# Optimization experiments

Hardware: AMD Instinct MI355X
Metric: run time of the kernel (lower is better)

Reference implementation:

```python
import jax, jax.numpy as jnp
import numpy as np

N = 16383        # complete binary tree, 14 levels
D_NODE = 512
D_SSM = 512
D_STATE = 16
MAX_DEPTH = 14   # number of BFS levels (depth 0..13)
LN_EPS = 1e-5


def setup_inputs() -> dict:
    key = jax.random.key(0)
    ks = jax.random.split(key, 8)
    # tree structure: parent[i] = (i-1)//2, root has parent -1; BFS order == index order
    parent = np.concatenate([np.array([-1]), (np.arange(1, N) - 1) // 2]).astype(np.int64)
    depth = np.floor(np.log2(np.arange(N) + 1)).astype(np.int32)
    s = jax.random.normal(ks[0], (N, D_NODE), jnp.float32)
    w = jax.random.uniform(ks[1], (N,), jnp.float32, minval=0.01, maxval=1.0)
    # parameters (xavier-ish scales)
    W_in = jax.random.normal(ks[2], (D_SSM, D_NODE + 1), jnp.float32) * (1.0 / np.sqrt(D_NODE + 1))
    b_in = jnp.zeros((D_SSM,), jnp.float32)
    W_delta = jax.random.normal(ks[3], (D_SSM, D_SSM), jnp.float32) * (1.0 / np.sqrt(D_SSM))
    # dt-style bias init: softplus(b) ~ dt in [1e-3, 1e-1]
    dt = jnp.exp(jax.random.uniform(ks[4], (D_SSM,), jnp.float32) * (np.log(0.1) - np.log(0.001)) + np.log(0.001))
    b_delta = dt + jnp.log(-jnp.expm1(-dt))
    W_w = jax.random.normal(ks[5], (D_SSM, 1), jnp.float32)
    b_w = jnp.zeros((D_SSM,), jnp.float32)
    A_log = jnp.log(jnp.broadcast_to(jnp.arange(1.0, D_STATE + 1.0, dtype=jnp.float32)[None, :], (D_SSM, D_STATE)))
    D = jnp.ones((D_SSM,), jnp.float32)
    W_B = jax.random.normal(ks[6], (D_STATE, D_SSM), jnp.float32) * (1.0 / np.sqrt(D_SSM))
    b_B = jnp.zeros((D_STATE,), jnp.float32)
    W_C = jax.random.normal(ks[7], (D_STATE, D_SSM), jnp.float32) * (1.0 / np.sqrt(D_SSM))
    b_C = jnp.zeros((D_STATE,), jnp.float32)
    gamma = jnp.ones((D_SSM,), jnp.float32)
    beta = jnp.zeros((D_SSM,), jnp.float32)
    return {"s": s, "w": w, "parent": jnp.asarray(parent), "depth": jnp.asarray(depth),
            "W_in": W_in, "b_in": b_in, "W_delta": W_delta, "b_delta": b_delta,
            "W_w": W_w, "b_w": b_w, "A_log": A_log, "D": D,
            "W_B": W_B, "b_B": b_B, "W_C": W_C, "b_C": b_C,
            "gamma": gamma, "beta": beta}


def reference(s, w, parent, depth, W_in, b_in, W_delta, b_delta, W_w, b_w,
              A_log, D, W_B, b_B, W_C, b_C, gamma, beta):
    n = s.shape[0]
    log_w = jnp.log(w + 1e-6)[:, None]                       # [N, 1]
    feat = jnp.concatenate([s, log_w], axis=1)               # [N, d_node+1]
    x = feat @ W_in.T + b_in                                 # [N, d_ssm]
    delta = jax.nn.softplus(x @ W_delta.T + b_delta) * jax.nn.sigmoid(log_w @ W_w.T + b_w)  # [N, d_ssm]
    A = -jnp.exp(A_log)                                      # [d_ssm, d_state]
    B = x @ W_B.T + b_B                                      # [N, d_state]
    C = x @ W_C.T + b_C                                      # [N, d_state]
    A_bar = jnp.exp(delta[:, :, None] * A[None])             # [N, d_ssm, d_state]
    Bx = (delta * x)[:, :, None] * B[:, None, :]             # [N, d_ssm, d_state]
    # level-parallel tree scan: all nodes at BFS depth l updated together
    par = jnp.maximum(parent, 0)
    has_par = (parent >= 0)[:, None, None]
    H = jnp.zeros((n, A_bar.shape[1], A_bar.shape[2]), x.dtype)
    for lvl in range(MAX_DEPTH):
        h_par = jnp.where(has_par, jnp.take(H, par, axis=0), 0.0)
        H = jnp.where((depth == lvl)[:, None, None], A_bar * h_par + Bx, H)
    Y = jnp.einsum('nds,ns->nd', H, C) + D * x               # [N, d_ssm]
    mu = jnp.mean(Y, axis=-1, keepdims=True)
    var = jnp.var(Y, axis=-1, keepdims=True)
    return (Y - mu) / jnp.sqrt(var + LN_EPS) * gamma + beta
```

## Files before the change

kernel.cpp:

```cpp
#include <hip/hip_runtime.h>
#include <hip/hip_bf16.h>
#include <math.h>

#define D_SSM 512
#define D_STATE 16
#define CKPT_BASE 511
#define CKPT_END 1023
#define N_CKPT 512
#define MPAD 16384

typedef __attribute__((ext_vector_type(8))) short short8;
typedef __attribute__((ext_vector_type(4))) float floatx4;

__device__ __forceinline__ unsigned short f2bf(float f) {
    unsigned int u = __float_as_uint(f);
    unsigned int r = (u + 0x7fffu + ((u >> 16) & 1u)) >> 16;
    return (unsigned short)r;
}
__device__ __forceinline__ float bf2f(unsigned short u) {
    return __uint_as_float(((unsigned int)u) << 16);
}
__device__ __forceinline__ void g2lds16(const void* g, void* l) {
    __builtin_amdgcn_global_load_lds(
        (const __attribute__((address_space(1))) void*)g,
        (__attribute__((address_space(3))) void*)l, 16, 0, 0);
}

__global__ __launch_bounds__(256) void prep_kernel(
    const float* __restrict__ s, const float* __restrict__ w,
    const float* __restrict__ W_in, const float* __restrict__ W_delta,
    const float* __restrict__ W_B, const float* __restrict__ W_C,
    unsigned short* __restrict__ s_bf, float* __restrict__ lw,
    unsigned short* __restrict__ Win_bf, unsigned short* __restrict__ Wd_bf,
    int Nn)
{
    const int b = blockIdx.x, t = threadIdx.x;
    if (b < MPAD) {
        unsigned int pack = 0;
        if (b < Nn) {
            float2 sv = *(const float2*)(s + (size_t)b * 512 + t * 2);
            pack = (unsigned int)f2bf(sv.x) | ((unsigned int)f2bf(sv.y) << 16);
        }
        *(unsigned int*)(s_bf + (size_t)b * 512 + t * 2) = pack;
        if (t == 0) lw[b] = (b < Nn) ? logf(w[b] + 1e-6f) : 0.f;
    } else if (b < MPAD + 512) {
        int c = b - MPAD;
        float a0 = W_in[(size_t)c * 513 + t * 2];
        float a1 = W_in[(size_t)c * 513 + t * 2 + 1];
        *(unsigned int*)(Win_bf + (size_t)c * 512 + t * 2) =
            (unsigned int)f2bf(a0) | ((unsigned int)f2bf(a1) << 16);
    } else if (b < MPAD + 1024) {
        int c = b - MPAD - 512;
        float2 wv = *(const float2*)(W_delta + (size_t)c * 512 + t * 2);
        *(unsigned int*)(Wd_bf + (size_t)c * 512 + t * 2) =
            (unsigned int)f2bf(wv.x) | ((unsigned int)f2bf(wv.y) << 16);
    } else {
        int c = b - MPAD - 1024;
        float2 wv; wv.x = 0.f; wv.y = 0.f;
        if (c < 16)      wv = *(const float2*)(W_B + (size_t)c * 512 + t * 2);
        else if (c < 32) wv = *(const float2*)(W_C + (size_t)(c - 16) * 512 + t * 2);
        *(unsigned int*)(Wd_bf + (size_t)(512 + c) * 512 + t * 2) =
            (unsigned int)f2bf(wv.x) | ((unsigned int)f2bf(wv.y) << 16);
    }
}

__global__ __launch_bounds__(256) void gemm_mfma(
    const unsigned short* __restrict__ Abf,
    const unsigned short* __restrict__ Wbf,
    float* __restrict__ outf,
    unsigned short* __restrict__ outbf,
    const float* __restrict__ bias,
    const float* __restrict__ lw,
    const float* __restrict__ wcol, int wcol_stride,
    const float* __restrict__ bw,
    const float* __restrict__ b_B, const float* __restrict__ b_C,
    float* __restrict__ Bm, float* __restrict__ Cm,
    int mode)
{
    __shared__ __align__(16) short As[2][128 * 32];
    __shared__ __align__(16) short Bs[2][128 * 32];
    const int tid = threadIdx.x;
    const int wave = tid >> 6, lane = tid & 63;
    const int row0 = blockIdx.y * 128;
    const int col0 = blockIdx.x * 128;
    const int wr = (wave >> 1) * 64;
    const int wc = (wave & 1) * 64;

    floatx4 acc[4][4] = {};

    const int srow = lane >> 2;
    const int sg   = (lane & 3) ^ ((srow >> 1) & 3);
    const int scol = sg * 8;

    const unsigned short* Ag = Abf + (size_t)(row0 + wave * 16 + srow) * 512 + scol;
    const unsigned short* Wg = Wbf + (size_t)(col0 + wave * 16 + srow) * 512 + scol;
    char* Al = (char*)&As[0][0] + wave * 1024;
    char* Bl = (char*)&Bs[0][0] + wave * 1024;

    #define STAGE(buf, k0)                                              \
        do {                                                            \
            g2lds16(Ag + (k0),            Al + (buf) * 8192);           \
            g2lds16(Ag + 64 * 512 + (k0), Al + (buf) * 8192 + 4096);    \
            g2lds16(Wg + (k0),            Bl + (buf) * 8192);           \
            g2lds16(Wg + 64 * 512 + (k0), Bl + (buf) * 8192 + 4096);    \
        } while (0)

    STAGE(0, 0);
    __syncthreads();

    for (int it = 0; it < 16; ++it) {
        const int cur = it & 1;
        if (it < 15) STAGE(cur ^ 1, (it + 1) * 32);

        short8 af[4], bfr[4];
        #pragma unroll
        for (int i = 0; i < 4; i++) {
            int m = wr + i * 16 + (lane & 15);
            int gm = (lane >> 4) ^ ((m >> 1) & 3);
            af[i] = *(const short8*)&As[cur][m * 32 + gm * 8];
        }
        #pragma unroll
        for (int j = 0; j < 4; j++) {
            int n = wc + j * 16 + (lane & 15);
            int gn = (lane >> 4) ^ ((n >> 1) & 3);
            bfr[j] = *(const short8*)&Bs[cur][n * 32 + gn * 8];
        }
        #pragma unroll
        for (int i = 0; i < 4; i++)
            #pragma unroll
            for (int j = 0; j < 4; j++)
                acc[i][j] = __builtin_amdgcn_mfma_f32_16x16x32_bf16(af[i], bfr[j], acc[i][j], 0, 0, 0);
        __syncthreads();
    }
    #undef STAGE

    if (col0 >= 512) {
        #pragma unroll
        for (int i = 0; i < 4; i++) {
            #pragma unroll
            for (int reg = 0; reg < 4; reg++) {
                int r = row0 + wr + i * 16 + (lane >> 4) * 4 + reg;
                #pragma unroll
                for (int j = 0; j < 4; j++) {
                    int c2 = wc + j * 16 + (lane & 15);
                    float z = acc[i][j][reg];
                    if (c2 < 16)      Bm[(size_t)r * 16 + c2]        = z + b_B[c2];
                    else if (c2 < 32) Cm[(size_t)r * 16 + (c2 - 16)] = z + b_C[c2 - 16];
                }
            }
        }
        return;
    }

    #pragma unroll
    for (int i = 0; i < 4; i++) {
        #pragma unroll
        for (int reg = 0; reg < 4; reg++) {
            int r = row0 + wr + i * 16 + (lane >> 4) * 4 + reg;
            float lwr = lw[r];
            #pragma unroll
            for (int j = 0; j < 4; j++) {
                int c = col0 + wc + j * 16 + (lane & 15);
                float z = acc[i][j][reg] + bias[c];
                if (mode == 0) {
                    float o = z + lwr * wcol[(size_t)c * wcol_stride];
                    outbf[(size_t)r * 512 + c] = f2bf(o);
                } else {
                    float sp = (z > 15.f) ? z : __logf(1.f + __expf(z));
                    float sg2 = __builtin_amdgcn_rcpf(1.f + __expf(-(lwr * wcol[c] + bw[c])));
                    outf[(size_t)r * 512 + c] = sp * sg2;
                }
            }
        }
    }
}

__device__ __forceinline__ bool geo_check(const float* As) {
    bool ok = true;
    #pragma unroll
    for (int s = 1; s < 16; s++) {
        float want = (float)(s + 1) * As[0];
        ok = ok && (fabsf(As[s] - want) <= 1e-4f * (float)(s + 1));
    }
    return ok;
}

__global__ __launch_bounds__(256) void ckpt_kernel(
    const unsigned short* __restrict__ x_bf, const float* __restrict__ delta,
    const float* __restrict__ Bm, const float* __restrict__ A_log,
    float* __restrict__ H9)
{
    const int n9 = blockIdx.x;
    const int t = threadIdx.x;
    const int d0 = t, d1 = t + 256;

    float As0[16], As1[16], acc0[16], acc1[16];
    #pragma unroll
    for (int s = 0; s < 16; s++) {
        As0[s] = -__expf(A_log[d0 * 16 + s]);
        As1[s] = -__expf(A_log[d1 * 16 + s]);
        acc0[s] = 0.f; acc1[s] = 0.f;
    }
    const bool fast = geo_check(As0) && geo_check(As1);

    float cum0 = 0.f, cum1 = 0.f;
    int a = CKPT_BASE + n9;
    while (a >= 0) {
        float da0 = delta[(size_t)a * 512 + d0];
        float da1 = delta[(size_t)a * 512 + d1];
        float bx0 = da0 * bf2f(x_bf[(size_t)a * 512 + d0]);
        float bx1 = da1 * bf2f(x_bf[(size_t)a * 512 + d1]);
        if (fast) {
            float r0 = __expf(As0[0] * cum0);
            float r1 = __expf(As1[0] * cum1);
            float pw0 = r0, pw1 = r1;
            #pragma unroll
            for (int s = 0; s < 16; s++) {
                float Bs = Bm[a * 16 + s];
                acc0[s] = fmaf(bx0 * pw0, Bs, acc0[s]);
                acc1[s] = fmaf(bx1 * pw1, Bs, acc1[s]);
                pw0 *= r0; pw1 *= r1;
            }
        } else {
            #pragma unroll
            for (int s = 0; s < 16; s++) {
                float Bs = Bm[a * 16 + s];
                acc0[s] = fmaf(bx0 * __expf(As0[s] * cum0), Bs, acc0[s]);
                acc1[s] = fmaf(bx1 * __expf(As1[s] * cum1), Bs, acc1[s]);
            }
        }
        cum0 += da0; cum1 += da1;
        a = (a - 1) >> 1;
    }

    float* p0 = H9 + ((size_t)n9 * 512 + d0) * 16;
    float* p1 = H9 + ((size_t)n9 * 512 + d1) * 16;
    #pragma unroll
    for (int s = 0; s < 16; s++) { p0[s] = acc0[s]; p1[s] = acc1[s]; }
}

__global__ __launch_bounds__(256) void scan_shallow(
    const unsigned short* __restrict__ x_bf, const float* __restrict__ delta,
    const float* __restrict__ Bm, const float* __restrict__ Cm,
    const float* __restrict__ A_log, const float* __restrict__ Dv,
    const float* __restrict__ gamma, const float* __restrict__ beta,
    float* __restrict__ out)
{
    const int n = blockIdx.x;
    const int t = threadIdx.x;
    const int d0 = t, d1 = t + 256;

    float As0[16], As1[16], acc0[16], acc1[16];
    #pragma unroll
    for (int s = 0; s < 16; s++) {
        As0[s] = -__expf(A_log[d0 * 16 + s]);
        As1[s] = -__expf(A_log[d1 * 16 + s]);
        acc0[s] = 0.f; acc1[s] = 0.f;
    }
    const bool fast = geo_check(As0) && geo_check(As1);

    float cum0 = 0.f, cum1 = 0.f;
    int a = n;
    while (a >= 0) {
        float da0 = delta[(size_t)a * 512 + d0];
        float da1 = delta[(size_t)a * 512 + d1];
        float bx0 = da0 * bf2f(x_bf[(size_t)a * 512 + d0]);
        float bx1 = da1 * bf2f(x_bf[(size_t)a * 512 + d1]);
        if (fast) {
            float r0 = __expf(As0[0] * cum0);
            float r1 = __expf(As1[0] * cum1);
            float pw0 = r0, pw1 = r1;
            #pragma unroll
            for (int s = 0; s < 16; s++) {
                float Bs = Bm[a * 16 + s];
                acc0[s] = fmaf(bx0 * pw0, Bs, acc0[s]);
                acc1[s] = fmaf(bx1 * pw1, Bs, acc1[s]);
                pw0 *= r0; pw1 *= r1;
            }
        } else {
            #pragma unroll
            for (int s = 0; s < 16; s++) {
                float Bs = Bm[a * 16 + s];
                acc0[s] = fmaf(bx0 * __expf(As0[s] * cum0), Bs, acc0[s]);
                acc1[s] = fmaf(bx1 * __expf(As1[s] * cum1), Bs, acc1[s]);
            }
        }
        cum0 += da0; cum1 += da1;
        a = (a - 1) >> 1;
    }

    float xn0 = bf2f(x_bf[(size_t)n * 512 + d0]);
    float xn1 = bf2f(x_bf[(size_t)n * 512 + d1]);
    float y0 = Dv[d0] * xn0, y1 = Dv[d1] * xn1;
    #pragma unroll
    for (int s = 0; s < 16; s++) {
        float Cs = Cm[(size_t)n * 16 + s];
        y0 += Cs * acc0[s];
        y1 += Cs * acc1[s];
    }

    float s1 = y0 + y1;
    float s2 = y0 * y0 + y1 * y1;
    #pragma unroll
    for (int off = 32; off > 0; off >>= 1) {
        s1 += __shfl_xor(s1, off);
        s2 += __shfl_xor(s2, off);
    }
    __shared__ float red[8];
    int wid = t >> 6, lane = t & 63;
    if (lane == 0) { red[wid] = s1; red[wid + 4] = s2; }
    __syncthreads();
    float S1 = red[0] + red[1] + red[2] + red[3];
    float S2 = red[4] + red[5] + red[6] + red[7];
    float mu = S1 * (1.f / 512.f);
    float var = S2 * (1.f / 512.f) - mu * mu;
    float inv = rsqrtf(var + 1e-5f);
    out[(size_t)n * 512 + d0] = (y0 - mu) * inv * gamma[d0] + beta[d0];
    out[(size_t)n * 512 + d1] = (y1 - mu) * inv * gamma[d1] + beta[d1];
}

__global__ __launch_bounds__(512) void scan_deep(
    const unsigned short* __restrict__ x_bf, const float* __restrict__ delta,
    const float* __restrict__ Bm, const float* __restrict__ Cm,
    const float* __restrict__ H9,
    const float* __restrict__ A_log, const float* __restrict__ Dv,
    const float* __restrict__ gamma, const float* __restrict__ beta,
    float* __restrict__ out)
{
    __shared__ float Y[31][512];
    __shared__ int nid[31];
    const int p = blockIdx.x;
    const int d = threadIdx.x;
    const int a9 = CKPT_BASE + p;

    float As0 = -__expf(A_log[d * 16]);
    bool fast = true;
    #pragma unroll
    for (int s = 1; s < 16; s++) {
        float As = -__expf(A_log[d * 16 + s]);
        fast = fast && (fabsf(As - (float)(s + 1) * As0) <= 1e-4f * (float)(s + 1));
    }

    float H9v[16];
    #pragma unroll
    for (int s = 0; s < 16; s++) H9v[s] = H9[((size_t)p * 512 + d) * 16 + s];

    {
        float xv = bf2f(x_bf[(size_t)a9 * 512 + d]);
        float y = Dv[d] * xv;
        #pragma unroll
        for (int s = 0; s < 16; s++) y = fmaf(Cm[(size_t)a9 * 16 + s], H9v[s], y);
        Y[0][d] = y;
        if (d == 0) nid[0] = a9;
    }

    auto step = [&](int n, const float* Hp, float* Hc, int slot) {
        float dlt = delta[(size_t)n * 512 + d];
        float xv = bf2f(x_bf[(size_t)n * 512 + d]);
        float bx = dlt * xv;
        const float* Bn = Bm + (size_t)n * 16;
        const float* Cn = Cm + (size_t)n * 16;
        float y = Dv[d] * xv;
        if (fast) {
            float r = __expf(As0 * dlt);
            float pw = r;
            #pragma unroll
            for (int s = 0; s < 16; s++) {
                Hc[s] = fmaf(pw, Hp[s], bx * Bn[s]);
                y = fmaf(Cn[s], Hc[s], y);
                pw *= r;
            }
        } else {
            #pragma unroll
            for (int s = 0; s < 16; s++) {
                float Ab = __expf(dlt * (-__expf(A_log[d * 16 + s])));
                Hc[s] = fmaf(Ab, Hp[s], bx * Bn[s]);
                y = fmaf(Cn[s], Hc[s], y);
            }
        }
        Y[slot][d] = y;
        if (d == 0) nid[slot] = n;
    };

    float H10[16], H11[16], H12[16], H13[16];
    int slot = 1;
    #pragma unroll
    for (int c0 = 0; c0 < 2; c0++) {
        int n10 = 2 * a9 + 1 + c0;
        step(n10, H9v, H10, slot++);
        #pragma unroll
        for (int c1 = 0; c1 < 2; c1++) {
            int n11 = 2 * n10 + 1 + c1;
            step(n11, H10, H11, slot++);
            #pragma unroll
            for (int c2 = 0; c2 < 2; c2++) {
                int n12 = 2 * n11 + 1 + c2;
                step(n12, H11, H12, slot++);
                #pragma unroll
                for (int c3 = 0; c3 < 2; c3++) {
                    int n13 = 2 * n12 + 1 + c3;
                    step(n13, H12, H13, slot++);
                }
            }
        }
    }
    __syncthreads();

    const int w = d >> 6, lane = d & 63;
    for (int i = w; i < 31; i += 8) {
        int n = nid[i];
        float v[8]; float s1 = 0.f, s2 = 0.f;
        #pragma unroll
        for (int k = 0; k < 8; k++) {
            v[k] = Y[i][lane + 64 * k];
            s1 += v[k]; s2 += v[k] * v[k];
        }
        #pragma unroll
        for (int off = 32; off > 0; off >>= 1) {
            s1 += __shfl_xor(s1, off);
            s2 += __shfl_xor(s2, off);
        }
        float mu = s1 * (1.f / 512.f);
        float inv = rsqrtf(s2 * (1.f / 512.f) - mu * mu + 1e-5f);
        #pragma unroll
        for (int k = 0; k < 8; k++) {
            int ch = lane + 64 * k;
            out[(size_t)n * 512 + ch] = (v[k] - mu) * inv * gamma[ch] + beta[ch];
        }
    }
}

extern "C" void kernel_launch(void* const* d_in, const int* in_sizes, int n_in,
                              void* d_out, int out_size, void* d_ws, size_t ws_size,
                              hipStream_t stream) {
    const float* s_in   = (const float*)d_in[0];
    const float* w      = (const float*)d_in[1];
    const float* W_in    = (const float*)d_in[4];
    const float* b_in    = (const float*)d_in[5];
    const float* W_delta = (const float*)d_in[6];
    const float* b_delta = (const float*)d_in[7];
    const float* W_w     = (const float*)d_in[8];
    const float* b_w     = (const float*)d_in[9];
    const float* A_log   = (const float*)d_in[10];
    const float* Dv      = (const float*)d_in[11];
    const float* W_B     = (const float*)d_in[12];
    const float* b_B     = (const float*)d_in[13];
    const float* W_C     = (const float*)d_in[14];
    const float* b_C     = (const float*)d_in[15];
    const float* gamma   = (const float*)d_in[16];
    const float* beta    = (const float*)d_in[17];
    float* out = (float*)d_out;

    const int Nn = in_sizes[1];

    float* ws    = (float*)d_ws;
    float* lw    = ws;
    float* delta = lw + MPAD;
    float* Bm    = delta + (size_t)MPAD * 512;
    float* Cm    = Bm + (size_t)MPAD * 16;
    float* H9    = Cm + (size_t)MPAD * 16;
    unsigned short* s_bf  = (unsigned short*)(H9 + (size_t)N_CKPT * 512 * 16);
    unsigned short* x_bf  = s_bf + (size_t)MPAD * 512;
    unsigned short* Win_bf = x_bf + (size_t)MPAD * 512;
    unsigned short* Wd_bf  = Win_bf + 512 * 512;

    prep_kernel<<<MPAD + 1024 + 128, 256, 0, stream>>>(s_in, w, W_in, W_delta, W_B, W_C,
                                                       s_bf, lw, Win_bf, Wd_bf, Nn);

    dim3 g1(4, 128);
    gemm_mfma<<<g1, 256, 0, stream>>>(s_bf, Win_bf, nullptr, x_bf,
                                      b_in, lw, W_in + 512, 513, nullptr,
                                      nullptr, nullptr, nullptr, nullptr, 0);
    dim3 g2(5, 128);
    gemm_mfma<<<g2, 256, 0, stream>>>(x_bf, Wd_bf, delta, nullptr,
                                      b_delta, lw, W_w, 1, b_w,
                                      b_B, b_C, Bm, Cm, 1);

    ckpt_kernel<<<N_CKPT, 256, 0, stream>>>(x_bf, delta, Bm, A_log, H9);

    scan_shallow<<<CKPT_BASE, 256, 0, stream>>>(x_bf, delta, Bm, Cm, A_log, Dv,
                                                gamma, beta, out);

    scan_deep<<<N_CKPT, 512, 0, stream>>>(x_bf, delta, Bm, Cm, H9, A_log, Dv,
                                          gamma, beta, out);
}
```

Measured before the change: 244.0 us.

## Fuse checkpoint computation into scan_deep and swizzle GEMM workgroup order

Removes the separate ckpt_kernel that wrote per-checkpoint states H9 to global memory; scan_deep now walks the ancestor chain itself to build the depth-9 state in registers. This drops one launch and the H9 write/read round trip (512x512x16 floats). Separately, the GEMM remaps block indices with an XCD-aware swizzle so neighbouring tiles land on the same chiplet for better L2 reuse. The fused path uses one thread per channel with 512 threads, so the ancestor walk's latency now sits in front of the deep scan rather than running as its own kernel.

```diff
diff --git a/kernel.cpp b/kernel.cpp
--- a/kernel.cpp
+++ b/kernel.cpp
@@ -5,7 +5,6 @@
 #define D_SSM 512
 #define D_STATE 16
 #define CKPT_BASE 511
-#define CKPT_END 1023
 #define N_CKPT 512
 #define MPAD 16384
 
@@ -81,8 +80,15 @@
     __shared__ __align__(16) short Bs[2][128 * 32];
     const int tid = threadIdx.x;
     const int wave = tid >> 6, lane = tid & 63;
-    const int row0 = blockIdx.y * 128;
-    const int col0 = blockIdx.x * 128;
+
+    const int nwg  = gridDim.x * gridDim.y;
+    const int orig = blockIdx.y * gridDim.x + blockIdx.x;
+    const int wsw  = (orig & 7) * (nwg >> 3) + (orig >> 3);
+    const int bx   = wsw % gridDim.x;
+    const int by   = wsw / gridDim.x;
+    const int row0 = by * 128;
+    const int col0 = bx * 128;
+
     const int wr = (wave >> 1) * 64;
     const int wc = (wave & 1) * 64;
 
@@ -185,60 +191,6 @@
     return ok;
 }
 
-__global__ __launch_bounds__(256) void ckpt_kernel(
-    const unsigned short* __restrict__ x_bf, const float* __restrict__ delta,
-    const float* __restrict__ Bm, const float* __restrict__ A_log,
-    float* __restrict__ H9)
-{
-    const int n9 = blockIdx.x;
-    const int t = threadIdx.x;
-    const int d0 = t, d1 = t + 256;
-
-    float As0[16], As1[16], acc0[16], acc1[16];
-    #pragma unroll
-    for (int s = 0; s < 16; s++) {
-        As0[s] = -__expf(A_log[d0 * 16 + s]);
-        As1[s] = -__expf(A_log[d1 * 16 + s]);
-        acc0[s] = 0.f; acc1[s] = 0.f;
-    }
-    const bool fast = geo_check(As0) && geo_check(As1);
-
-    float cum0 = 0.f, cum1 = 0.f;
-    int a = CKPT_BASE + n9;
-    while (a >= 0) {
-        float da0 = delta[(size_t)a * 512 + d0];
-        float da1 = delta[(size_t)a * 512 + d1];
-        float bx0 = da0 * bf2f(x_bf[(size_t)a * 512 + d0]);
-        float bx1 = da1 * bf2f(x_bf[(size_t)a * 512 + d1]);
-        if (fast) {
-            float r0 = __expf(As0[0] * cum0);
-            float r1 = __expf(As1[0] * cum1);
-            float pw0 = r0, pw1 = r1;
-            #pragma unroll
-            for (int s = 0; s < 16; s++) {
-                float Bs = Bm[a * 16 + s];
-                acc0[s] = fmaf(bx0 * pw0, Bs, acc0[s]);
-                acc1[s] = fmaf(bx1 * pw1, Bs, acc1[s]);
-                pw0 *= r0; pw1 *= r1;
-            }
-        } else {
-            #pragma unroll
-            for (int s = 0; s < 16; s++) {
-                float Bs = Bm[a * 16 + s];
-                acc0[s] = fmaf(bx0 * __expf(As0[s] * cum0), Bs, acc0[s]);
-                acc1[s] = fmaf(bx1 * __expf(As1[s] * cum1), Bs, acc1[s]);
-            }
-        }
-        cum0 += da0; cum1 += da1;
-        a = (a - 1) >> 1;
-    }
-
-    float* p0 = H9 + ((size_t)n9 * 512 + d0) * 16;
-    float* p1 = H9 + ((size_t)n9 * 512 + d1) * 16;
-    #pragma unroll
-    for (int s = 0; s < 16; s++) { p0[s] = acc0[s]; p1[s] = acc1[s]; }
-}
-
 __global__ __launch_bounds__(256) void scan_shallow(
     const unsigned short* __restrict__ x_bf, const float* __restrict__ delta,
     const float* __restrict__ Bm, const float* __restrict__ Cm,
@@ -322,7 +274,6 @@
 __global__ __launch_bounds__(512) void scan_deep(
     const unsigned short* __restrict__ x_bf, const float* __restrict__ delta,
     const float* __restrict__ Bm, const float* __restrict__ Cm,
-    const float* __restrict__ H9,
     const float* __restrict__ A_log, const float* __restrict__ Dv,
     const float* __restrict__ gamma, const float* __restrict__ beta,
     float* __restrict__ out)
@@ -343,7 +294,32 @@
 
     float H9v[16];
     #pragma unroll
-    for (int s = 0; s < 16; s++) H9v[s] = H9[((size_t)p * 512 + d) * 16 + s];
+    for (int s = 0; s < 16; s++) H9v[s] = 0.f;
+    {
+        float cum = 0.f;
+        int a = a9;
+        while (a >= 0) {
+            float da = delta[(size_t)a * 512 + d];
+            float bx = da * bf2f(x_bf[(size_t)a * 512 + d]);
+            if (fast) {
+                float r = __expf(As0 * cum);
+                float pw = r;
+                #pragma unroll
+                for (int s = 0; s < 16; s++) {
+                    H9v[s] = fmaf(bx * pw, Bm[a * 16 + s], H9v[s]);
+                    pw *= r;
+                }
+            } else {
+                #pragma unroll
+                for (int s = 0; s < 16; s++) {
+                    float As = -__expf(A_log[d * 16 + s]);
+                    H9v[s] = fmaf(bx * __expf(As * cum), Bm[a * 16 + s], H9v[s]);
+                }
+            }
+            cum += da;
+            a = (a - 1) >> 1;
+        }
+    }
 
     {
         float xv = bf2f(x_bf[(size_t)a9 * 512 + d]);
@@ -458,8 +434,7 @@
     float* delta = lw + MPAD;
     float* Bm    = delta + (size_t)MPAD * 512;
     float* Cm    = Bm + (size_t)MPAD * 16;
-    float* H9    = Cm + (size_t)MPAD * 16;
-    unsigned short* s_bf  = (unsigned short*)(H9 + (size_t)N_CKPT * 512 * 16);
+    unsigned short* s_bf  = (unsigned short*)(Cm + (size_t)MPAD * 16);
     unsigned short* x_bf  = s_bf + (size_t)MPAD * 512;
     unsigned short* Win_bf = x_bf + (size_t)MPAD * 512;
     unsigned short* Wd_bf  = Win_bf + 512 * 512;
@@ -476,11 +451,9 @@
                                       b_delta, lw, W_w, 1, b_w,
                                       b_B, b_C, Bm, Cm, 1);
 
-    ckpt_kernel<<<N_CKPT, 256, 0, stream>>>(x_bf, delta, Bm, A_log, H9);
-
     scan_shallow<<<CKPT_BASE, 256, 0, stream>>>(x_bf, delta, Bm, Cm, A_log, Dv,
                                                 gamma, beta, out);
 
-    scan_deep<<<N_CKPT, 512, 0, stream>>>(x_bf, delta, Bm, Cm, H9, A_log, Dv,
+    scan_deep<<<N_CKPT, 512, 0, stream>>>(x_bf, delta, Bm, Cm, A_log, Dv,
                                           gamma, beta, out);
 }
```

Measured after the change: 225.6 us. 1.08x faster.
